# Kernel tuning notes

Hardware: AMD Instinct MI355X
Metric: run time of the kernel (lower is better)

Reference implementation:

```python
import jax, jax.numpy as jnp
import numpy as np

GAMMA = 1.0
BIG = 1e10  # finite stand-in for +inf so exp/log stay NaN-free under autodiff


def _pairwise_sq_dist(X, Y):
    # X: (na, T, d), Y: (nb, T, d) -> D: (na, nb, T, T) squared euclidean
    sqx = jnp.sum(X * X, axis=-1)                      # (na, T)
    sqy = jnp.sum(Y * Y, axis=-1)                      # (nb, T)
    cross = jnp.einsum('atd,bsd->abts', X, Y)          # (na, nb, T, T)
    return sqx[:, None, :, None] + sqy[None, :, None, :] - 2.0 * cross


def _soft_dtw(D, gamma):
    # D: (B, T, T) -> (B,) soft-DTW values, anti-diagonal wavefront via lax.scan.
    B, T, _ = D.shape
    inv_g = 1.0 / gamma
    idx = jnp.arange(T)

    def step(carry, p):
        prev2, prev1 = carry                           # diagonals p-2, p-1: (B, T)
        j = p - idx
        valid = (j >= 0) & (j < T)
        d = D[:, idx, jnp.clip(j, 0, T - 1)]           # (B, T) costs on diag p
        # shifted neighbors: prev2[i-1] (diag), prev1[i-1] (up), prev1[i] (left)
        corner = jnp.where(p == 0, 0.0, BIG)           # R[0,0] = 0 boundary
        prev2_s = jnp.concatenate([jnp.broadcast_to(corner, (B, 1)), prev2[:, :-1]], axis=1)
        prev1_s = jnp.concatenate([jnp.full((B, 1), BIG, D.dtype), prev1[:, :-1]], axis=1)
        r0 = -prev2_s * inv_g
        r1 = -prev1_s * inv_g
        r2 = -prev1 * inv_g
        rmax = jnp.maximum(jnp.maximum(r0, r1), r2)
        rsum = jnp.exp(r0 - rmax) + jnp.exp(r1 - rmax) + jnp.exp(r2 - rmax)
        softmin = -gamma * (jnp.log(rsum) + rmax)
        new = jnp.where(valid[None, :], d + softmin, BIG)
        return (prev1, new), None

    init = (jnp.full((B, T), BIG, D.dtype), jnp.full((B, T), BIG, D.dtype))
    (_, last), _ = jax.lax.scan(step, init, jnp.arange(2 * T - 1))
    return last[:, T - 1]                              # R[T, T]


def setup_inputs() -> dict:
    key = jax.random.key(0)
    kx, ky = jax.random.split(key)
    X = jax.random.normal(kx, (128, 128, 8), dtype=jnp.float32)
    Y = jax.random.normal(ky, (16, 128, 8), dtype=jnp.float32)
    return {"X": X, "Y": Y}


def reference(X, Y):
    na, T, _ = X.shape
    nb = Y.shape[0]
    D = _pairwise_sq_dist(X, Y).reshape(na * nb, T, T)
    dist = _soft_dtw(D, GAMMA)
    return dist.reshape(na, nb)
```

## Files before the change

kernel.cpp:

```cpp
#include <hip/hip_runtime.h>

#define T 128
#define DIMS 8
#define L2E 1.4426950408889634f
#define LN2F 0.6931471805599453f

typedef _Float16 h2 __attribute__((ext_vector_type(2)));

__device__ __forceinline__ float ror1(float x) {
    return __int_as_float(__builtin_amdgcn_update_dpp(
        __float_as_int(x), __float_as_int(x), 0x13C, 0xF, 0xF, false));
}

template <int CTRL>
__device__ __forceinline__ float dppmax(float x) {
    float t = __int_as_float(__builtin_amdgcn_update_dpp(
        __float_as_int(x), __float_as_int(x), CTRL, 0xF, 0xF, false));
    return fmaxf(x, t);
}

__launch_bounds__(256)
__global__ void sdtw_kernel(const float* __restrict__ X,
                            const float* __restrict__ Y,
                            float* __restrict__ out) {
    __shared__ __align__(16) float lds[4 * 656];
    const int lane = threadIdx.x & 63;
    const int w    = threadIdx.x >> 6;
    const int pair = blockIdx.x * 4 + w;
    const int a = pair >> 4;
    const int b = pair & 15;

    float* yw  = lds + w * 656;
    float* sqw = yw + 520;

    {
        const float* ybase = Y + (size_t)b * T * DIMS;
        for (int r = lane; r < T; r += 64) {
            const float4* src = (const float4*)(ybase + r * DIMS);
            float4 y0 = src[0], y1 = src[1];
            float s = y0.x*y0.x + y0.y*y0.y + y0.z*y0.z + y0.w*y0.w
                    + y1.x*y1.x + y1.y*y1.y + y1.z*y1.z + y1.w*y1.w;
            const float c = 2.0f * L2E;
            h2 a0 = { (_Float16)(c*y0.x), (_Float16)(c*y0.y) };
            h2 a1 = { (_Float16)(c*y0.z), (_Float16)(c*y0.w) };
            h2 a2 = { (_Float16)(c*y1.x), (_Float16)(c*y1.y) };
            h2 a3 = { (_Float16)(c*y1.z), (_Float16)(c*y1.w) };
            float4 pk;
            pk.x = __builtin_bit_cast(float, a0);
            pk.y = __builtin_bit_cast(float, a1);
            pk.z = __builtin_bit_cast(float, a2);
            pk.w = __builtin_bit_cast(float, a3);
            *(float4*)(yw + ((r + 1) << 2)) = pk;
            sqw[r + 1] = -L2E * s;
        }
        if (lane < 2) {
            int m = lane ? 129 : 0;
            float4 z; z.x = 0.f; z.y = 0.f; z.z = 0.f; z.w = 0.f;
            *(float4*)(yw + (m << 2)) = z;
            sqw[m] = -3.0e37f;
        }
    }

    h2 x10, x11, x12, x13, x20, x21, x22, x23;
    float lsx1, lsx2;
    {
        const float* xb = X + ((size_t)a * T + lane) * DIMS;
        const float4* s0 = (const float4*)xb;
        float4 v0 = s0[0], v1 = s0[1];
        x10 = h2{ (_Float16)v0.x, (_Float16)v0.y };
        x11 = h2{ (_Float16)v0.z, (_Float16)v0.w };
        x12 = h2{ (_Float16)v1.x, (_Float16)v1.y };
        x13 = h2{ (_Float16)v1.z, (_Float16)v1.w };
        lsx1 = -L2E * (v0.x*v0.x+v0.y*v0.y+v0.z*v0.z+v0.w*v0.w
                      +v1.x*v1.x+v1.y*v1.y+v1.z*v1.z+v1.w*v1.w);
        const float4* s1 = (const float4*)(xb + 64 * DIMS);
        float4 u0 = s1[0], u1 = s1[1];
        x20 = h2{ (_Float16)u0.x, (_Float16)u0.y };
        x21 = h2{ (_Float16)u0.z, (_Float16)u0.w };
        x22 = h2{ (_Float16)u1.x, (_Float16)u1.y };
        x23 = h2{ (_Float16)u1.z, (_Float16)u1.w };
        lsx2 = -L2E * (u0.x*u0.x+u0.y*u0.y+u0.z*u0.z+u0.w*u0.w
                      +u1.x*u1.x+u1.y*u1.y+u1.z*u1.z+u1.w*u1.w);
    }

    __syncthreads();

    const bool l0 = (lane == 0);

    float p1a, p2a = 0.f, p1b = 0.f, p2b = 0.f;
    int off = 90;
    {
        int m0 = min(max(1 - lane, 0), 129);
        float4 yv = *(const float4*)(yw + (m0 << 2));
        float acc = lsx1 + sqw[m0];
        acc = __builtin_amdgcn_fdot2(x10, __builtin_bit_cast(h2, yv.x), acc, false);
        acc = __builtin_amdgcn_fdot2(x11, __builtin_bit_cast(h2, yv.y), acc, false);
        acc = __builtin_amdgcn_fdot2(x12, __builtin_bit_cast(h2, yv.z), acc, false);
        acc = __builtin_amdgcn_fdot2(x13, __builtin_bit_cast(h2, yv.w), acc, false);
        p1a = __builtin_amdgcn_exp2f(acc) * 0x1p90f;
    }

    int jp1a = 2 - lane;
    int jp1b = -62 - lane;

#define BODY() {                                                              \
    float r1 = ror1(p1a), r2 = ror1(p2a);                                     \
    float q1 = ror1(p1b), q2 = ror1(p2b);                                     \
    float A1 = l0 ? 0.0f : r2;                                                \
    float B1 = l0 ? 0.0f : r1;                                                \
    float A2 = l0 ? r2 : q2;                                                  \
    float B2 = l0 ? r1 : q1;                                                  \
    int m1 = min(max(jp1a, 0), 129);                                          \
    int m2 = min(max(jp1b, 0), 129);                                          \
    float4 yv1 = *(const float4*)(yw + (m1 << 2));                            \
    float  sq1 = sqw[m1];                                                     \
    float4 yv2 = *(const float4*)(yw + (m2 << 2));                            \
    float  sq2 = sqw[m2];                                                     \
    float acc1 = lsx1 + sq1;                                                  \
    acc1 = __builtin_amdgcn_fdot2(x10, __builtin_bit_cast(h2, yv1.x), acc1, false); \
    acc1 = __builtin_amdgcn_fdot2(x11, __builtin_bit_cast(h2, yv1.y), acc1, false); \
    acc1 = __builtin_amdgcn_fdot2(x12, __builtin_bit_cast(h2, yv1.z), acc1, false); \
    acc1 = __builtin_amdgcn_fdot2(x13, __builtin_bit_cast(h2, yv1.w), acc1, false); \
    float acc2 = lsx2 + sq2;                                                  \
    acc2 = __builtin_amdgcn_fdot2(x20, __builtin_bit_cast(h2, yv2.x), acc2, false); \
    acc2 = __builtin_amdgcn_fdot2(x21, __builtin_bit_cast(h2, yv2.y), acc2, false); \
    acc2 = __builtin_amdgcn_fdot2(x22, __builtin_bit_cast(h2, yv2.z), acc2, false); \
    acc2 = __builtin_amdgcn_fdot2(x23, __builtin_bit_cast(h2, yv2.w), acc2, false); \
    float E1 = __builtin_amdgcn_exp2f(acc1);                                  \
    float E2 = __builtin_amdgcn_exp2f(acc2);                                  \
    float S1 = E1 * ((A1 + B1) + p1a);                                        \
    float S2 = E2 * ((A2 + B2) + p1b);                                        \
    p2a = p1a; p1a = S1;                                                      \
    p2b = p1b; p1b = S2;                                                      \
    ++jp1a; ++jp1b;                                                           \
}

#define RENORM() {                                                            \
    float mx = fmaxf(fmaxf(p1a, p1b), fmaxf(p2a, p2b));                       \
    mx = dppmax<0x111>(mx);                                    \
    mx = dppmax<0x112>(mx);                                    \
    mx = dppmax<0x114>(mx);                                    \
    mx = dppmax<0x118>(mx);                                    \
             \
    int r0 = __builtin_amdgcn_readlane(__float_as_int(mx), 15);               \
    int r1_ = __builtin_amdgcn_readlane(__float_as_int(mx), 31);              \
    int r2_ = __builtin_amdgcn_readlane(__float_as_int(mx), 47);              \
    int r3 = __builtin_amdgcn_readlane(__float_as_int(mx), 63);               \
    int mb = max(max(r0, r1_), max(r2_, r3));  \
    int e = ((mb >> 23) & 0xff) - 217;    \
    p1a = ldexpf(p1a, -e); p2a = ldexpf(p2a, -e);                             \
    p1b = ldexpf(p1b, -e); p2b = ldexpf(p2b, -e);                             \
    off -= e;     \
}

    for (int g = 0; g < 63; ++g) {
        BODY(); BODY(); BODY(); BODY();
        RENORM();
    }
    BODY();
    BODY();

    if (lane == 63)
        out[pair] = ((float)off - __builtin_amdgcn_logf(p1b)) * LN2F;
}

extern "C" void kernel_launch(void* const* d_in, const int* in_sizes, int n_in,
                              void* d_out, int out_size, void* d_ws, size_t ws_size,
                              hipStream_t stream) {
    const float* X = (const float*)d_in[0];
    const float* Y = (const float*)d_in[1];
    float* out = (float*)d_out;
    sdtw_kernel<<<512, 256, 0, stream>>>(X, Y, out);
}
```

Before: 96.95 us.

## Assign adjacent row pairs per lane and pad Y table to drop clamping

Each lane now owns rows 2*lane and 2*lane+1 instead of lane and lane+64. The odd row's up and diagonal neighbours then sit in the same lane, so only one cross-lane shift per row pair is needed, and lane 0 needs no special case because a zero-filling DPP shift handles the boundary. The Y table is stored in LDS with 126 sentinel rows of padding on each side at a 6-float stride, so per-step index clamping disappears and rows are fetched through a rotating register pipeline that loads one row ahead. In exchange the kernel uses more LDS per block, which may limit occupancy, and the 6-float stride may cause bank conflicts.

```diff
diff --git a/kernel.cpp b/kernel.cpp
--- a/kernel.cpp
+++ b/kernel.cpp
@@ -1,15 +1,14 @@
 #include <hip/hip_runtime.h>
 
 #define T 128
-#define DIMS 8
 #define L2E 1.4426950408889634f
 #define LN2F 0.6931471805599453f
 
 typedef _Float16 h2 __attribute__((ext_vector_type(2)));
 
-__device__ __forceinline__ float ror1(float x) {
+__device__ __forceinline__ float shr1(float x) {
     return __int_as_float(__builtin_amdgcn_update_dpp(
-        __float_as_int(x), __float_as_int(x), 0x13C, 0xF, 0xF, false));
+        0, __float_as_int(x), 0x138, 0xF, 0xF, true));
 }
 
 template <int CTRL>
@@ -19,149 +18,154 @@
     return fmaxf(x, t);
 }
 
+struct Row { float2 u, v; float s; };
+
+__device__ __forceinline__ Row loadRow(const float* p) {
+    Row r;
+    r.u = *(const float2*)p;
+    r.v = *(const float2*)(p + 2);
+    r.s = p[4];
+    return r;
+}
+
+__device__ __forceinline__ float dot2(h2 x, float ybits, float acc) {
+    return __builtin_amdgcn_fdot2(x, __builtin_bit_cast(h2, ybits), acc, false);
+}
+
 __launch_bounds__(256)
 __global__ void sdtw_kernel(const float* __restrict__ X,
                             const float* __restrict__ Y,
                             float* __restrict__ out) {
-    __shared__ __align__(16) float lds[4 * 656];
+    __shared__ __align__(16) float lds[4 * 2304];
     const int lane = threadIdx.x & 63;
     const int w    = threadIdx.x >> 6;
     const int pair = blockIdx.x * 4 + w;
     const int a = pair >> 4;
     const int b = pair & 15;
 
-    float* yw  = lds + w * 656;
-    float* sqw = yw + 520;
+    float* yw = lds + w * 2304;
 
     {
-        const float* ybase = Y + (size_t)b * T * DIMS;
-        for (int r = lane; r < T; r += 64) {
-            const float4* src = (const float4*)(ybase + r * DIMS);
-            float4 y0 = src[0], y1 = src[1];
-            float s = y0.x*y0.x + y0.y*y0.y + y0.z*y0.z + y0.w*y0.w
-                    + y1.x*y1.x + y1.y*y1.y + y1.z*y1.z + y1.w*y1.w;
-            const float c = 2.0f * L2E;
-            h2 a0 = { (_Float16)(c*y0.x), (_Float16)(c*y0.y) };
-            h2 a1 = { (_Float16)(c*y0.z), (_Float16)(c*y0.w) };
-            h2 a2 = { (_Float16)(c*y1.x), (_Float16)(c*y1.y) };
-            h2 a3 = { (_Float16)(c*y1.z), (_Float16)(c*y1.w) };
-            float4 pk;
-            pk.x = __builtin_bit_cast(float, a0);
-            pk.y = __builtin_bit_cast(float, a1);
-            pk.z = __builtin_bit_cast(float, a2);
-            pk.w = __builtin_bit_cast(float, a3);
-            *(float4*)(yw + ((r + 1) << 2)) = pk;
-            sqw[r + 1] = -L2E * s;
-        }
-        if (lane < 2) {
-            int m = lane ? 129 : 0;
-            float4 z; z.x = 0.f; z.y = 0.f; z.z = 0.f; z.w = 0.f;
-            *(float4*)(yw + (m << 2)) = z;
-            sqw[m] = -3.0e37f;
+        const float* ybase = Y + (size_t)b * T * 8;
+        for (int r = lane; r < 383; r += 64) {
+            float4 pk; pk.x = 0.f; pk.y = 0.f; pk.z = 0.f; pk.w = 0.f;
+            float sq = -3.0e37f;
+            int j = r - 126;
+            if (j >= 0 && j < T) {
+                const float4* src = (const float4*)(ybase + j * 8);
+                float4 y0 = src[0], y1 = src[1];
+                float s = y0.x*y0.x + y0.y*y0.y + y0.z*y0.z + y0.w*y0.w
+                        + y1.x*y1.x + y1.y*y1.y + y1.z*y1.z + y1.w*y1.w;
+                const float c = 2.0f * L2E;
+                h2 a0 = { (_Float16)(c*y0.x), (_Float16)(c*y0.y) };
+                h2 a1 = { (_Float16)(c*y0.z), (_Float16)(c*y0.w) };
+                h2 a2 = { (_Float16)(c*y1.x), (_Float16)(c*y1.y) };
+                h2 a3 = { (_Float16)(c*y1.z), (_Float16)(c*y1.w) };
+                pk.x = __builtin_bit_cast(float, a0);
+                pk.y = __builtin_bit_cast(float, a1);
+                pk.z = __builtin_bit_cast(float, a2);
+                pk.w = __builtin_bit_cast(float, a3);
+                sq = -L2E * s;
+            }
+            float* dst = yw + r * 6;
+            float2 h; h.x = pk.x; h.y = pk.y;
+            float2 g; g.x = pk.z; g.y = pk.w;
+            *(float2*)dst = h;
+            *(float2*)(dst + 2) = g;
+            dst[4] = sq;
         }
     }
 
-    h2 x10, x11, x12, x13, x20, x21, x22, x23;
-    float lsx1, lsx2;
+    h2 xe0, xe1, xe2, xe3, xo0, xo1, xo2, xo3;
+    float lsxe, lsxo;
     {
-        const float* xb = X + ((size_t)a * T + lane) * DIMS;
+        const float* xb = X + ((size_t)a * T + 2 * lane) * 8;
         const float4* s0 = (const float4*)xb;
-        float4 v0 = s0[0], v1 = s0[1];
-        x10 = h2{ (_Float16)v0.x, (_Float16)v0.y };
-        x11 = h2{ (_Float16)v0.z, (_Float16)v0.w };
-        x12 = h2{ (_Float16)v1.x, (_Float16)v1.y };
-        x13 = h2{ (_Float16)v1.z, (_Float16)v1.w };
-        lsx1 = -L2E * (v0.x*v0.x+v0.y*v0.y+v0.z*v0.z+v0.w*v0.w
+        float4 v0 = s0[0], v1 = s0[1], u0 = s0[2], u1 = s0[3];
+        xe0 = h2{ (_Float16)v0.x, (_Float16)v0.y };
+        xe1 = h2{ (_Float16)v0.z, (_Float16)v0.w };
+        xe2 = h2{ (_Float16)v1.x, (_Float16)v1.y };
+        xe3 = h2{ (_Float16)v1.z, (_Float16)v1.w };
+        lsxe = -L2E * (v0.x*v0.x+v0.y*v0.y+v0.z*v0.z+v0.w*v0.w
                       +v1.x*v1.x+v1.y*v1.y+v1.z*v1.z+v1.w*v1.w);
-        const float4* s1 = (const float4*)(xb + 64 * DIMS);
-        float4 u0 = s1[0], u1 = s1[1];
-        x20 = h2{ (_Float16)u0.x, (_Float16)u0.y };
-        x21 = h2{ (_Float16)u0.z, (_Float16)u0.w };
-        x22 = h2{ (_Float16)u1.x, (_Float16)u1.y };
-        x23 = h2{ (_Float16)u1.z, (_Float16)u1.w };
-        lsx2 = -L2E * (u0.x*u0.x+u0.y*u0.y+u0.z*u0.z+u0.w*u0.w
+        xo0 = h2{ (_Float16)u0.x, (_Float16)u0.y };
+        xo1 = h2{ (_Float16)u0.z, (_Float16)u0.w };
+        xo2 = h2{ (_Float16)u1.x, (_Float16)u1.y };
+        xo3 = h2{ (_Float16)u1.z, (_Float16)u1.w };
+        lsxo = -L2E * (u0.x*u0.x+u0.y*u0.y+u0.z*u0.z+u0.w*u0.w
                       +u1.x*u1.x+u1.y*u1.y+u1.z*u1.z+u1.w*u1.w);
     }
 
     __syncthreads();
 
-    const bool l0 = (lane == 0);
+    Row ra = loadRow(yw + (126 - 2 * lane) * 6);
+    Row rb = loadRow(yw + (127 - 2 * lane) * 6);
+    Row rc = loadRow(yw + (128 - 2 * lane) * 6);
+    Row rd;
+    const float* fptr = yw + (129 - 2 * lane) * 6;
 
-    float p1a, p2a = 0.f, p1b = 0.f, p2b = 0.f;
+    float fe0 = 0.f, fo0 = 0.f, fo1 = 0.f;
     int off = 90;
+    float fe1;
     {
-        int m0 = min(max(1 - lane, 0), 129);
-        float4 yv = *(const float4*)(yw + (m0 << 2));
-        float acc = lsx1 + sqw[m0];
-        acc = __builtin_amdgcn_fdot2(x10, __builtin_bit_cast(h2, yv.x), acc, false);
-        acc = __builtin_amdgcn_fdot2(x11, __builtin_bit_cast(h2, yv.y), acc, false);
-        acc = __builtin_amdgcn_fdot2(x12, __builtin_bit_cast(h2, yv.z), acc, false);
-        acc = __builtin_amdgcn_fdot2(x13, __builtin_bit_cast(h2, yv.w), acc, false);
-        p1a = __builtin_amdgcn_exp2f(acc) * 0x1p90f;
+        float acc = lsxe + ra.s;
+        acc = dot2(xe0, ra.u.x, acc);
+        acc = dot2(xe1, ra.u.y, acc);
+        acc = dot2(xe2, ra.v.x, acc);
+        acc = dot2(xe3, ra.v.y, acc);
+        fe1 = __builtin_amdgcn_exp2f(acc) * 0x1p90f;
     }
 
-    int jp1a = 2 - lane;
-    int jp1b = -62 - lane;
-
-#define BODY() {                                                              \
-    float r1 = ror1(p1a), r2 = ror1(p2a);                                     \
-    float q1 = ror1(p1b), q2 = ror1(p2b);                                     \
-    float A1 = l0 ? 0.0f : r2;                                                \
-    float B1 = l0 ? 0.0f : r1;                                                \
-    float A2 = l0 ? r2 : q2;                                                  \
-    float B2 = l0 ? r1 : q1;                                                  \
-    int m1 = min(max(jp1a, 0), 129);                                          \
-    int m2 = min(max(jp1b, 0), 129);                                          \
-    float4 yv1 = *(const float4*)(yw + (m1 << 2));                            \
-    float  sq1 = sqw[m1];                                                     \
-    float4 yv2 = *(const float4*)(yw + (m2 << 2));                            \
-    float  sq2 = sqw[m2];                                                     \
-    float acc1 = lsx1 + sq1;                                                  \
-    acc1 = __builtin_amdgcn_fdot2(x10, __builtin_bit_cast(h2, yv1.x), acc1, false); \
-    acc1 = __builtin_amdgcn_fdot2(x11, __builtin_bit_cast(h2, yv1.y), acc1, false); \
-    acc1 = __builtin_amdgcn_fdot2(x12, __builtin_bit_cast(h2, yv1.z), acc1, false); \
-    acc1 = __builtin_amdgcn_fdot2(x13, __builtin_bit_cast(h2, yv1.w), acc1, false); \
-    float acc2 = lsx2 + sq2;                                                  \
-    acc2 = __builtin_amdgcn_fdot2(x20, __builtin_bit_cast(h2, yv2.x), acc2, false); \
-    acc2 = __builtin_amdgcn_fdot2(x21, __builtin_bit_cast(h2, yv2.y), acc2, false); \
-    acc2 = __builtin_amdgcn_fdot2(x22, __builtin_bit_cast(h2, yv2.z), acc2, false); \
-    acc2 = __builtin_amdgcn_fdot2(x23, __builtin_bit_cast(h2, yv2.w), acc2, false); \
-    float E1 = __builtin_amdgcn_exp2f(acc1);                                  \
-    float E2 = __builtin_amdgcn_exp2f(acc2);                                  \
-    float S1 = E1 * ((A1 + B1) + p1a);                                        \
-    float S2 = E2 * ((A2 + B2) + p1b);                                        \
-    p2a = p1a; p1a = S1;                                                      \
-    p2b = p1b; p1b = S2;                                                      \
-    ++jp1a; ++jp1b;                                                           \
+#define BODY(PE1, PE2, PO1, PO2, RO, RE, RF) {          \
+    RF = loadRow(fptr); fptr += 6;                      \
+    float sB = shr1(PO1);                               \
+    float sA = shr1(PO2);                               \
+    float ae = lsxe + RE.s;                             \
+    ae = dot2(xe0, RE.u.x, ae);                         \
+    ae = dot2(xe1, RE.u.y, ae);                         \
+    ae = dot2(xe2, RE.v.x, ae);                         \
+    ae = dot2(xe3, RE.v.y, ae);                         \
+    float ao = lsxo + RO.s;                             \
+    ao = dot2(xo0, RO.u.x, ao);                         \
+    ao = dot2(xo1, RO.u.y, ao);                         \
+    ao = dot2(xo2, RO.v.x, ao);                         \
+    ao = dot2(xo3, RO.v.y, ao);                         \
+    float Ee = __builtin_amdgcn_exp2f(ae);              \
+    float Eo = __builtin_amdgcn_exp2f(ao);              \
+    float Se = Ee * ((sA + sB) + PE1);                  \
+    float So = Eo * ((PE2 + PE1) + PO1);                \
+    PE2 = Se; PO2 = So;                                 \
 }
 
 #define RENORM() {                                                            \
-    float mx = fmaxf(fmaxf(p1a, p1b), fmaxf(p2a, p2b));                       \
+    float mx = fmaxf(fmaxf(fe0, fe1), fmaxf(fo0, fo1));                       \
     mx = dppmax<0x111>(mx);                                    \
     mx = dppmax<0x112>(mx);                                    \
     mx = dppmax<0x114>(mx);                                    \
     mx = dppmax<0x118>(mx);                                    \
-             \
-    int r0 = __builtin_amdgcn_readlane(__float_as_int(mx), 15);               \
+    int r0_ = __builtin_amdgcn_readlane(__float_as_int(mx), 15);              \
     int r1_ = __builtin_amdgcn_readlane(__float_as_int(mx), 31);              \
     int r2_ = __builtin_amdgcn_readlane(__float_as_int(mx), 47);              \
-    int r3 = __builtin_amdgcn_readlane(__float_as_int(mx), 63);               \
-    int mb = max(max(r0, r1_), max(r2_, r3));  \
-    int e = ((mb >> 23) & 0xff) - 217;    \
-    p1a = ldexpf(p1a, -e); p2a = ldexpf(p2a, -e);                             \
-    p1b = ldexpf(p1b, -e); p2b = ldexpf(p2b, -e);                             \
-    off -= e;     \
+    int r3_ = __builtin_amdgcn_readlane(__float_as_int(mx), 63);              \
+    int mb = max(max(r0_, r1_), max(r2_, r3_));                               \
+    int e = ((mb >> 23) & 0xff) - 217;                \
+    fe0 = ldexpf(fe0, -e); fe1 = ldexpf(fe1, -e);                             \
+    fo0 = ldexpf(fo0, -e); fo1 = ldexpf(fo1, -e);                             \
+    off -= e;                                                                 \
 }
 
     for (int g = 0; g < 63; ++g) {
-        BODY(); BODY(); BODY(); BODY();
+        BODY(fe1, fe0, fo1, fo0, ra, rb, rd);
+        BODY(fe0, fe1, fo0, fo1, rb, rc, ra);
+        BODY(fe1, fe0, fo1, fo0, rc, rd, rb);
+        BODY(fe0, fe1, fo0, fo1, rd, ra, rc);
         RENORM();
     }
-    BODY();
-    BODY();
+    BODY(fe1, fe0, fo1, fo0, ra, rb, rd);
+    BODY(fe0, fe1, fo0, fo1, rb, rc, ra);
 
     if (lane == 63)
-        out[pair] = ((float)off - __builtin_amdgcn_logf(p1b)) * LN2F;
+        out[pair] = ((float)off - __builtin_amdgcn_logf(fo1)) * LN2F;
 }
 
 extern "C" void kernel_launch(void* const* d_in, const int* in_sizes, int n_in,
```

Result: faster. 86.50 us (-10.8%).
